# Kernel tuning notes

Measured on AMD Instinct MI355X. Metric: run time of the kernel, lower is better.

Reference implementation:

```python
import jax, jax.numpy as jnp
import numpy as np

Z, DIM_IN, DIM_TS, DIM_OUT = 4096, 256, 2048, 256


def setup_inputs() -> dict:
    key = jax.random.key(0)
    k1, k2, k3 = jax.random.split(key, 3)
    features = jax.random.normal(k1, (Z, DIM_IN), dtype=jnp.float32)
    # Dense stand-in for the sparse CG buffer T: [dim_ts, dim_in * dim_in]
    T = jax.random.normal(k2, (DIM_TS, DIM_IN * DIM_IN), dtype=jnp.float32) * 0.02
    # KernelLinear output (learned mixing weights): [dim_out, dim_ts]
    W = jax.random.normal(k3, (DIM_OUT, DIM_TS), dtype=jnp.float32) * 0.02
    return {"features": features, "T": T, "W": W}


def reference(features, T, W):
    # features: [..., dim_in]; flatten leading dims as in the torch module
    *size, n = features.shape
    x = features.reshape(-1, n)                       # [z, i]
    # (T.t() @ W.T).T == W @ T ; reshape to [k, i, j]
    K = (W @ T).reshape(W.shape[0], n, n)             # [k, i, j]
    # per-sample bilinear (quadratic) form
    out = jnp.einsum('kij,zi,zj->zk', K, x, x)        # [z, k]
    return out.reshape(*size, -1)
```

## Files before the change

kernel.cpp:

```cpp
#include <hip/hip_runtime.h>

#define ZDIM 4096
#define DIN  256
#define DTS  2048
#define DOUT 256
#define CDIM 65536
#define SPLIT 8
#define CHUNK (CDIM / SPLIT)

typedef float fv4 __attribute__((ext_vector_type(4)));
typedef __bf16 bv8 __attribute__((ext_vector_type(8)));
typedef unsigned short u16;
typedef u16 uv8 __attribute__((ext_vector_type(8)));
typedef u16 uv4 __attribute__((ext_vector_type(4)));

union BC  { __bf16 b; u16 u; };
union VC8 { uv8 u; bv8 b; };

static __device__ __forceinline__ u16  f2b(float f){ BC c; c.b=(__bf16)f; return c.u; }
static __device__ __forceinline__ float b2f(u16 v){ BC c; c.u=v; return (float)c.b; }
static __device__ __forceinline__ bv8  asb(uv8 x){ VC8 c; c.u=x; return c.b; }
static __device__ __forceinline__ uv8  pack8(fv4 a, fv4 b){
  uv8 p;
  p[0]=f2b(a[0]); p[1]=f2b(a[1]); p[2]=f2b(a[2]); p[3]=f2b(a[3]);
  p[4]=f2b(b[0]); p[5]=f2b(b[1]); p[6]=f2b(b[2]); p[7]=f2b(b[3]);
  return p;
}

__global__ __launch_bounds__(512, 2) void k_wt(const float* __restrict__ W,
                                               const float* __restrict__ T,
                                               u16* __restrict__ Km) {
  __shared__ u16 Al[256 * 40];
  __shared__ u16 Bl[32 * 128];
  const int tid  = threadIdx.x;
  const int lane = tid & 63;
  const int wave = tid >> 6;
  const int wk = (wave >> 1) * 64;
  const int wc = (wave & 1) * 64;
  const int cb = blockIdx.x * 128;
  const int ar = lane & 15, tg = lane >> 4;

  fv4 acc[4][4];
#pragma unroll
  for (int m = 0; m < 4; ++m)
#pragma unroll
    for (int n = 0; n < 4; ++n)
#pragma unroll
      for (int r = 0; r < 4; ++r) acc[m][n][r] = 0.f;

  for (int t0 = 0; t0 < DTS; t0 += 32) {
#pragma unroll
    for (int p = 0; p < 2; ++p) {
      int oct = tid + p * 512;
      int kr = oct >> 2, ts = (oct & 3) * 8;
      const float* src = W + (size_t)kr * DTS + t0 + ts;
      fv4 a = *(const fv4*)src, b = *(const fv4*)(src + 4);
      *(uv8*)&Al[kr * 40 + ts] = pack8(a, b);
    }
    {
      int tr = tid >> 4, co = (tid & 15) * 8;
      const float* src = T + (size_t)(t0 + tr) * CDIM + cb + co;
      fv4 a = *(const fv4*)src, b = *(const fv4*)(src + 4);
      *(uv8*)&Bl[tr * 128 + co] = pack8(a, b);
    }
    __syncthreads();
    bv8 af[4];
#pragma unroll
    for (int m = 0; m < 4; ++m)
      af[m] = asb(*(const uv8*)&Al[(wk + m * 16 + ar) * 40 + tg * 8]);
#pragma unroll
    for (int n = 0; n < 4; ++n) {
      uv8 bu;
#pragma unroll
      for (int e = 0; e < 8; ++e)
        bu[e] = Bl[(tg * 8 + e) * 128 + wc + n * 16 + ar];
      bv8 bf = asb(bu);
#pragma unroll
      for (int m = 0; m < 4; ++m)
        acc[m][n] = __builtin_amdgcn_mfma_f32_16x16x32_bf16(af[m], bf, acc[m][n], 0, 0, 0);
    }
    __syncthreads();
  }
#pragma unroll
  for (int m = 0; m < 4; ++m)
#pragma unroll
    for (int n = 0; n < 4; ++n)
#pragma unroll
      for (int r = 0; r < 4; ++r) {
        int kr = wk + m * 16 + tg * 4 + r;
        int cc = cb + wc + n * 16 + ar;
        Km[(size_t)kr * CDIM + cc] = f2b(acc[m][n][r]);
      }
}

__global__ __launch_bounds__(512, 4) void k_bil(const float* __restrict__ X,
                                                const u16* __restrict__ Km,
                                                float* __restrict__ P) {
  __shared__ u16 Xl[64 * 264];
  __shared__ u16 Ol[64 * 40];
  __shared__ u16 Bl[256 * 40];
  const int tid  = threadIdx.x;
  const int lane = tid & 63;
  const int wave = tid >> 6;
  const int wkk  = wave * 32;
  const int bid  = blockIdx.x;
  const int s    = bid & 7;
  const int z0   = (bid >> 3) * 64;
  const int cs   = s * CHUNK;
  const int ar = lane & 15, tg = lane >> 4;

  for (int idx = tid; idx < 64 * 32; idx += 512) {
    int row = idx >> 5, sg = (idx & 31) * 8;
    const float* src = X + (size_t)(z0 + row) * DIN + sg;
    fv4 a = *(const fv4*)src, b = *(const fv4*)(src + 4);
    *(uv8*)&Xl[row * 264 + sg] = pack8(a, b);
  }
  __syncthreads();

  fv4 acc[4][2];
#pragma unroll
  for (int m = 0; m < 4; ++m)
#pragma unroll
    for (int n = 0; n < 2; ++n)
#pragma unroll
      for (int r = 0; r < 4; ++r) acc[m][n][r] = 0.f;

  const int zr  = tid & 63;
  const int oc  = (tid >> 6) * 4;
  const int kks = tid >> 2;
  const int qq  = (tid & 3) * 8;

  for (int cc = 0; cc < CHUNK; cc += 32) {
    int cg = cs + cc;
    int i  = cg >> 8, j0 = cg & 255;
    {
      float xi = b2f(Xl[zr * 264 + i]);
      uv4 xj = *(const uv4*)&Xl[zr * 264 + j0 + oc];
      uv4 o;
#pragma unroll
      for (int e = 0; e < 4; ++e) o[e] = f2b(xi * b2f(xj[e]));
      *(uv4*)&Ol[zr * 40 + oc] = o;
    }
#pragma unroll
    for (int p = 0; p < 2; ++p) {
      int kk = kks + p * 128;
      uv8 v = *(const uv8*)&Km[(size_t)kk * CDIM + cg + qq];
      *(uv8*)&Bl[kk * 40 + qq] = v;
    }
    __syncthreads();
    bv8 af[4], bf[2];
#pragma unroll
    for (int m = 0; m < 4; ++m)
      af[m] = asb(*(const uv8*)&Ol[(m * 16 + ar) * 40 + tg * 8]);
#pragma unroll
    for (int n = 0; n < 2; ++n)
      bf[n] = asb(*(const uv8*)&Bl[(wkk + n * 16 + ar) * 40 + tg * 8]);
#pragma unroll
    for (int n = 0; n < 2; ++n)
#pragma unroll
      for (int m = 0; m < 4; ++m)
        acc[m][n] = __builtin_amdgcn_mfma_f32_16x16x32_bf16(af[m], bf[n], acc[m][n], 0, 0, 0);
    __syncthreads();
  }
  float* dst = P + (size_t)s * (ZDIM * DOUT) + (size_t)z0 * DOUT;
#pragma unroll
  for (int m = 0; m < 4; ++m)
#pragma unroll
    for (int n = 0; n < 2; ++n)
#pragma unroll
      for (int r = 0; r < 4; ++r)
        dst[(size_t)(m * 16 + tg * 4 + r) * DOUT + wkk + n * 16 + ar] = acc[m][n][r];
}

__global__ __launch_bounds__(256) void k_red(const float* __restrict__ P,
                                             float* __restrict__ O) {
  size_t idx = ((size_t)blockIdx.x * 256 + threadIdx.x) * 4;
  fv4 acc;
#pragma unroll
  for (int r = 0; r < 4; ++r) acc[r] = 0.f;
#pragma unroll
  for (int p = 0; p < SPLIT; ++p)
    acc += *(const fv4*)&P[(size_t)p * (ZDIM * DOUT) + idx];
  *(fv4*)&O[idx] = acc;
}

extern "C" void kernel_launch(void* const* d_in, const int* in_sizes, int n_in,
                              void* d_out, int out_size, void* d_ws, size_t ws_size,
                              hipStream_t stream) {
  const float* feat = (const float*)d_in[0];
  const float* T    = (const float*)d_in[1];
  const float* W    = (const float*)d_in[2];
  float* out = (float*)d_out;

  u16*   Km = (u16*)d_ws;
  float* P  = (float*)((char*)d_ws + (size_t)DOUT * CDIM * 2);

  k_wt <<<dim3(512),  dim3(512), 0, stream>>>(W, T, Km);
  k_bil<<<dim3(512),  dim3(512), 0, stream>>>(feat, Km, P);
  k_red<<<dim3(1024), dim3(256), 0, stream>>>(P, out);
}
```

Baseline: 394.3 us.

## Factor x_i out of bilinear GEMM, keep x_j fragments in registers, double-buffer K via LDS DMA

The bilinear kernel no longer builds the bf16 outer-product tile x_i*x_j in LDS every step. It keeps the bf16 x_j A-fragments in registers for all 256 j and runs the MFMAs against K for each i into a temporary accumulator. That accumulator is then scaled by fp32 x_i and added into the main accumulator. K tiles are streamed with global_load_lds into a double-buffered LDS tile, so the load of the next tile overlaps the current MFMAs, and one of the two barriers per step is removed. This costs many more registers, with launch bounds dropped to 2 blocks per CU, plus an extra multiply-add pass every 8 steps. Precision also changes slightly, since x_i is now applied in fp32 instead of being rounded into the bf16 product.

```diff
diff --git a/kernel.cpp b/kernel.cpp
--- a/kernel.cpp
+++ b/kernel.cpp
@@ -18,7 +18,6 @@
 union VC8 { uv8 u; bv8 b; };
 
 static __device__ __forceinline__ u16  f2b(float f){ BC c; c.b=(__bf16)f; return c.u; }
-static __device__ __forceinline__ float b2f(u16 v){ BC c; c.u=v; return (float)c.b; }
 static __device__ __forceinline__ bv8  asb(uv8 x){ VC8 c; c.u=x; return c.b; }
 static __device__ __forceinline__ uv8  pack8(fv4 a, fv4 b){
   uv8 p;
@@ -93,12 +92,11 @@
       }
 }
 
-__global__ __launch_bounds__(512, 4) void k_bil(const float* __restrict__ X,
+__global__ __launch_bounds__(512, 2) void k_bil(const float* __restrict__ X,
                                                 const u16* __restrict__ Km,
                                                 float* __restrict__ P) {
-  __shared__ u16 Xl[64 * 264];
-  __shared__ u16 Ol[64 * 40];
-  __shared__ u16 Bl[256 * 40];
+  __shared__ u16 Bl[2][256 * 32];
+  __shared__ float Xt[32 * 64];
   const int tid  = threadIdx.x;
   const int lane = tid & 63;
   const int wave = tid >> 6;
@@ -106,70 +104,92 @@
   const int bid  = blockIdx.x;
   const int s    = bid & 7;
   const int z0   = (bid >> 3) * 64;
+  const int i0   = s * 32;
   const int cs   = s * CHUNK;
   const int ar = lane & 15, tg = lane >> 4;
 
-  for (int idx = tid; idx < 64 * 32; idx += 512) {
-    int row = idx >> 5, sg = (idx & 31) * 8;
-    const float* src = X + (size_t)(z0 + row) * DIN + sg;
-    fv4 a = *(const fv4*)src, b = *(const fv4*)(src + 4);
-    *(uv8*)&Xl[row * 264 + sg] = pack8(a, b);
-  }
+  for (int idx = tid; idx < 32 * 64; idx += 512) {
+    int ii = idx >> 6, z = idx & 63;
+    Xt[idx] = X[(size_t)(z0 + z) * DIN + i0 + ii];
+  }
+
+  uv8 af[4][8];
+#pragma unroll
+  for (int m = 0; m < 4; ++m) {
+    const float* row = X + (size_t)(z0 + m * 16 + ar) * DIN;
+#pragma unroll
+    for (int js = 0; js < 8; ++js) {
+      const float* src = row + js * 32 + tg * 8;
+      fv4 a = *(const fv4*)src, b = *(const fv4*)(src + 4);
+      af[m][js] = pack8(a, b);
+    }
+  }
+
+#define STAGE(BUF, CBASE)                                                        \
+  {                                                                              \
+    _Pragma("unroll")                                                            \
+    for (int p = 0; p < 2; ++p) {                                                \
+      int idx = p * 512 + tid;                                                   \
+      int kk = idx >> 2;                                                         \
+      int jj = (idx & 3) * 8;                                                    \
+      const u16* gsrc = Km + (size_t)kk * CDIM + (CBASE) + jj;                   \
+      u16* ldst = &Bl[BUF][idx * 8];                                             \
+      __builtin_amdgcn_global_load_lds(                                          \
+          (const __attribute__((address_space(1))) void*)gsrc,                   \
+          (__attribute__((address_space(3))) void*)ldst, 16, 0, 0);              \
+    }                                                                            \
+  }
+
+  STAGE(0, cs)
   __syncthreads();
 
-  fv4 acc[4][2];
+  fv4 mas[4][2], aci[4][2];
 #pragma unroll
   for (int m = 0; m < 4; ++m)
 #pragma unroll
     for (int n = 0; n < 2; ++n)
 #pragma unroll
-      for (int r = 0; r < 4; ++r) acc[m][n][r] = 0.f;
-
-  const int zr  = tid & 63;
-  const int oc  = (tid >> 6) * 4;
-  const int kks = tid >> 2;
-  const int qq  = (tid & 3) * 8;
-
-  for (int cc = 0; cc < CHUNK; cc += 32) {
-    int cg = cs + cc;
-    int i  = cg >> 8, j0 = cg & 255;
-    {
-      float xi = b2f(Xl[zr * 264 + i]);
-      uv4 xj = *(const uv4*)&Xl[zr * 264 + j0 + oc];
-      uv4 o;
-#pragma unroll
-      for (int e = 0; e < 4; ++e) o[e] = f2b(xi * b2f(xj[e]));
-      *(uv4*)&Ol[zr * 40 + oc] = o;
-    }
-#pragma unroll
-    for (int p = 0; p < 2; ++p) {
-      int kk = kks + p * 128;
-      uv8 v = *(const uv8*)&Km[(size_t)kk * CDIM + cg + qq];
-      *(uv8*)&Bl[kk * 40 + qq] = v;
-    }
-    __syncthreads();
-    bv8 af[4], bf[2];
-#pragma unroll
-    for (int m = 0; m < 4; ++m)
-      af[m] = asb(*(const uv8*)&Ol[(m * 16 + ar) * 40 + tg * 8]);
+      for (int r = 0; r < 4; ++r) { mas[m][n][r] = 0.f; aci[m][n][r] = 0.f; }
+
+  int buf = 0;
+  for (int i = 0; i < 32; ++i) {
+#pragma unroll
+    for (int js = 0; js < 8; ++js) {
+      const int st = i * 8 + js;
+      if (st + 1 < 256) STAGE(buf ^ 1, cs + (st + 1) * 32)
+      bv8 bf[2];
+#pragma unroll
+      for (int n = 0; n < 2; ++n)
+        bf[n] = asb(*(const uv8*)&Bl[buf][(wkk + n * 16 + ar) * 32 + tg * 8]);
+#pragma unroll
+      for (int n = 0; n < 2; ++n)
+#pragma unroll
+        for (int m = 0; m < 4; ++m)
+          aci[m][n] = __builtin_amdgcn_mfma_f32_16x16x32_bf16(asb(af[m][js]), bf[n], aci[m][n], 0, 0, 0);
+      __syncthreads();
+      buf ^= 1;
+    }
+#pragma unroll
+    for (int m = 0; m < 4; ++m) {
+      fv4 xi4 = *(const fv4*)&Xt[i * 64 + m * 16 + tg * 4];
+#pragma unroll
+      for (int n = 0; n < 2; ++n) {
+        mas[m][n] += xi4 * aci[m][n];
+#pragma unroll
+        for (int r = 0; r < 4; ++r) aci[m][n][r] = 0.f;
+      }
+    }
+  }
+#undef STAGE
+
+  float* dst = P + (size_t)s * (ZDIM * DOUT) + (size_t)z0 * DOUT;
+#pragma unroll
+  for (int m = 0; m < 4; ++m)
 #pragma unroll
     for (int n = 0; n < 2; ++n)
-      bf[n] = asb(*(const uv8*)&Bl[(wkk + n * 16 + ar) * 40 + tg * 8]);
-#pragma unroll
-    for (int n = 0; n < 2; ++n)
-#pragma unroll
-      for (int m = 0; m < 4; ++m)
-        acc[m][n] = __builtin_amdgcn_mfma_f32_16x16x32_bf16(af[m], bf[n], acc[m][n], 0, 0, 0);
-    __syncthreads();
-  }
-  float* dst = P + (size_t)s * (ZDIM * DOUT) + (size_t)z0 * DOUT;
-#pragma unroll
-  for (int m = 0; m < 4; ++m)
-#pragma unroll
-    for (int n = 0; n < 2; ++n)
 #pragma unroll
       for (int r = 0; r < 4; ++r)
-        dst[(size_t)(m * 16 + tg * 4 + r) * DOUT + wkk + n * 16 + ar] = acc[m][n][r];
+        dst[(size_t)(m * 16 + tg * 4 + r) * DOUT + wkk + n * 16 + ar] = mas[m][n][r];
 }
 
 __global__ __launch_bounds__(256) void k_red(const float* __restrict__ P,
```

Result: slower. 432.1 us (+9.6%).
